# Performance work log

Hardware: AMD Instinct MI355X
Metric: run time of the kernel (lower is better)

Reference implementation:

```python
import jax, jax.numpy as jnp
import numpy as np

N_NODES = 100000
N_EDGES = 1600000
IN_C, HID, OUT_C = 128, 128, 64
BN_EPS = 1e-5


def gcn_conv(x, W, b, src, dst):
    # PyG GCNConv(normalize=False): linear first, then sum-aggregate over edges
    m = x @ W                                   # [N, out_dim]
    agg = jax.ops.segment_sum(m[src], dst, num_segments=N_NODES)  # scatter-add by dst
    return agg + b


def batch_norm(h, gamma, beta):
    mu = jnp.mean(h, axis=0)
    var = jnp.var(h, axis=0)
    return (h - mu) * jax.lax.rsqrt(var + BN_EPS) * gamma + beta


def setup_inputs() -> dict:
    key = jax.random.key(0)
    ks = jax.random.split(key, 8)
    x = jax.random.normal(ks[0], (N_NODES, IN_C), dtype=jnp.float32)
    edge_src = jax.random.randint(ks[1], (N_EDGES,), 0, N_NODES, dtype=jnp.int32)
    edge_dst = jnp.sort(jax.random.randint(ks[2], (N_EDGES,), 0, N_NODES, dtype=jnp.int32))
    def glorot(k, shape):
        lim = float(np.sqrt(6.0 / (shape[0] + shape[1])))
        return jax.random.uniform(k, shape, jnp.float32, -lim, lim)
    return {
        "x": x, "edge_src": edge_src, "edge_dst": edge_dst,
        "W0": glorot(ks[3], (IN_C, HID)), "b0": jnp.zeros((HID,), jnp.float32),
        "W1": glorot(ks[4], (HID, HID)), "b1": jnp.zeros((HID,), jnp.float32),
        "W2": glorot(ks[5], (HID, OUT_C)), "b2": jnp.zeros((OUT_C,), jnp.float32),
        "g0": jnp.ones((HID,), jnp.float32), "be0": jnp.zeros((HID,), jnp.float32),
        "g1": jnp.ones((HID,), jnp.float32), "be1": jnp.zeros((HID,), jnp.float32),
    }


def reference(x, edge_src, edge_dst, W0, b0, W1, b1, W2, b2, g0, be0, g1, be1):
    # layer 0: conv -> BN -> residual (dims match: 128==128) -> ReLU (dropout p=0)
    h = gcn_conv(x, W0, b0, edge_src, edge_dst)
    h = batch_norm(h, g0, be0)
    h = h + x  # residual, in_channels == hidden_channels
    x1 = jax.nn.relu(h)
    # layer 1
    h = gcn_conv(x1, W1, b1, edge_src, edge_dst)
    h = batch_norm(h, g1, be1)
    h = h + x1
    x2 = jax.nn.relu(h)
    # final layer: conv only
    return gcn_conv(x2, W2, b2, edge_src, edge_dst)
```

## Files before the change

kernel.cpp:

```cpp
#include <hip/hip_runtime.h>

#define BN_EPS 1e-5f

typedef __attribute__((ext_vector_type(8))) short bf16x8;
typedef __attribute__((ext_vector_type(4))) float f32x4;

__device__ __forceinline__ short f2bf(float f) {
    union { float f; unsigned u; } v; v.f = f;
    unsigned r = (v.u + 0x7fffu + ((v.u >> 16) & 1u)) >> 16;
    return (short)r;
}
__device__ __forceinline__ float bflo(unsigned d) {
    union { unsigned u; float f; } v; v.u = d << 16; return v.f;
}
__device__ __forceinline__ float bfhi(unsigned d) {
    union { unsigned u; float f; } v; v.u = d & 0xffff0000u; return v.f;
}

__global__ __launch_bounds__(256) void build_off_k(const int* __restrict__ dst,
                                                   int* __restrict__ off, int E, int N) {
    int i = blockIdx.x * 256 + threadIdx.x;
    if (i > E) return;
    int cur  = (i < E) ? dst[i] : N;
    int prev = (i == 0) ? -1 : dst[i - 1];
    for (int n = prev + 1; n <= cur; ++n) off[n] = i;
}

__global__ void zero_k(float* p, int n) {
    int i = blockIdx.x * blockDim.x + threadIdx.x;
    if (i < n) p[i] = 0.f;
}

__global__ __launch_bounds__(256) void wtrans_k(const float* __restrict__ W,
                                                short* __restrict__ Wt, int K, int C) {
    int i = blockIdx.x * 256 + threadIdx.x;
    if (i >= K * C) return;
    int c = i / K, k = i % K;
    Wt[i] = f2bf(W[k * C + c]);
}

template <int OUTC, int MODE>
__global__ __launch_bounds__(256) void mgemm_k(const void* __restrict__ Xp,
                                               const short* __restrict__ Wt,
                                               short* __restrict__ M,
                                               const float* __restrict__ ss,
                                               const void* __restrict__ Rp,
                                               short* __restrict__ X1, int N) {
    constexpr int NR = OUTC / 16;
    __shared__ short sW[OUTC][136];

    const int tid = threadIdx.x;
    for (int q = tid; q < OUTC * 16; q += 256) {
        int r = q >> 4, s = q & 15;
        *(int4*)&sW[r][s * 8] = ((const int4*)Wt)[q];
    }
    __syncthreads();

    const int wave = tid >> 6, lane = tid & 63;
    const int lr = lane & 15, lg = lane >> 4;
    const int row0 = blockIdx.x * 128 + wave * 32;

    f32x4 acc[2][NR];
    #pragma unroll
    for (int m = 0; m < 2; ++m)
        #pragma unroll
        for (int n = 0; n < NR; ++n) acc[m][n] = (f32x4){0.f, 0.f, 0.f, 0.f};

    #pragma unroll
    for (int kk = 0; kk < 4; ++kk) {
        bf16x8 a[2];
        const int ch0 = kk * 32 + lg * 8;
        #pragma unroll
        for (int m = 0; m < 2; ++m) {
            int row = row0 + m * 16 + lr;
            float v[8] = {0.f, 0.f, 0.f, 0.f, 0.f, 0.f, 0.f, 0.f};
            if (row < N) {
                if constexpr (MODE == 0) {
                    const float4* p = (const float4*)((const float*)Xp + (size_t)row * 128 + ch0);
                    float4 h0 = p[0], h1 = p[1];
                    v[0] = h0.x; v[1] = h0.y; v[2] = h0.z; v[3] = h0.w;
                    v[4] = h1.x; v[5] = h1.y; v[6] = h1.z; v[7] = h1.w;
                } else {
                    int4 hb = *(const int4*)((const short*)Xp + (size_t)row * 128 + ch0);
                    v[0] = bflo(hb.x); v[1] = bfhi(hb.x);
                    v[2] = bflo(hb.y); v[3] = bfhi(hb.y);
                    v[4] = bflo(hb.z); v[5] = bfhi(hb.z);
                    v[6] = bflo(hb.w); v[7] = bfhi(hb.w);
                    float4 sc0 = *(const float4*)&ss[ch0];
                    float4 sc1 = *(const float4*)&ss[ch0 + 4];
                    float4 sh0 = *(const float4*)&ss[128 + ch0];
                    float4 sh1 = *(const float4*)&ss[128 + ch0 + 4];
                    float sc[8] = {sc0.x, sc0.y, sc0.z, sc0.w, sc1.x, sc1.y, sc1.z, sc1.w};
                    float sh[8] = {sh0.x, sh0.y, sh0.z, sh0.w, sh1.x, sh1.y, sh1.z, sh1.w};
                    float r[8];
                    if constexpr (MODE == 1) {
                        const float4* rp = (const float4*)((const float*)Rp + (size_t)row * 128 + ch0);
                        float4 r0 = rp[0], r1 = rp[1];
                        r[0] = r0.x; r[1] = r0.y; r[2] = r0.z; r[3] = r0.w;
                        r[4] = r1.x; r[5] = r1.y; r[6] = r1.z; r[7] = r1.w;
                    } else {
                        int4 rb = *(const int4*)((const short*)Rp + (size_t)row * 128 + ch0);
                        r[0] = bflo(rb.x); r[1] = bfhi(rb.x);
                        r[2] = bflo(rb.y); r[3] = bfhi(rb.y);
                        r[4] = bflo(rb.z); r[5] = bfhi(rb.z);
                        r[6] = bflo(rb.w); r[7] = bfhi(rb.w);
                    }
                    #pragma unroll
                    for (int k = 0; k < 8; ++k)
                        v[k] = fmaxf(fmaf(v[k], sc[k], sh[k]) + r[k], 0.f);
                }
            }
            #pragma unroll
            for (int k = 0; k < 8; ++k) a[m][k] = f2bf(v[k]);
            if constexpr (MODE == 1) {
                if (row < N) *(bf16x8*)&X1[(size_t)row * 128 + ch0] = a[m];
            }
        }
        #pragma unroll
        for (int n = 0; n < NR; ++n) {
            bf16x8 b = *(const bf16x8*)&sW[n * 16 + lr][kk * 32 + lg * 8];
            acc[0][n] = __builtin_amdgcn_mfma_f32_16x16x32_bf16(a[0], b, acc[0][n], 0, 0, 0);
            acc[1][n] = __builtin_amdgcn_mfma_f32_16x16x32_bf16(a[1], b, acc[1][n], 0, 0, 0);
        }
    }

    #pragma unroll
    for (int m = 0; m < 2; ++m)
        #pragma unroll
        for (int r = 0; r < 4; ++r) {
            int row = row0 + m * 16 + lg * 4 + r;
            if (row < N) {
                #pragma unroll
                for (int n = 0; n < NR; ++n)
                    M[(size_t)row * OUTC + n * 16 + lr] = f2bf(acc[m][n][r]);
            }
        }
}

template <int C, bool STATS, bool OUTBF>
__global__ __launch_bounds__(256) void agg_k(const short* __restrict__ M,
                                             const int* __restrict__ src,
                                             const int* __restrict__ off,
                                             const float* __restrict__ bias,
                                             void* __restrict__ Hp,
                                             float* __restrict__ stats, int N) {
    constexpr int T = C / 8;
    constexpr int G = 64 / T;
    const int wave = threadIdx.x >> 6, lane = threadIdx.x & 63;
    const int g = lane / T, t = lane % T;
    const uint4* __restrict__ Mq = (const uint4*)M;

    float sum[8], sq[8];
    if constexpr (STATS) {
        #pragma unroll
        for (int k = 0; k < 8; ++k) { sum[k] = 0.f; sq[k] = 0.f; }
    }

    for (int node = blockIdx.x * 4 + wave; node < N; node += gridDim.x * 4) {
        const int e0 = off[node], e1 = off[node + 1];
        float acc[8];
        #pragma unroll
        for (int k = 0; k < 8; ++k) acc[k] = 0.f;

        for (int base = e0; base < e1; base += 64) {
            int cnt = e1 - base; if (cnt > 64) cnt = 64;
            int s = (base + lane < e1) ? src[base + lane] : 0;
            int ngrp = (cnt + G - 1) / G;
            for (int j = 0; j < ngrp; j += 4) {
                int i0 = j * G + g, i1 = i0 + G, i2 = i0 + 2 * G, i3 = i0 + 3 * G;
                int s0 = __shfl(s, i0 & 63), s1 = __shfl(s, i1 & 63);
                int s2 = __shfl(s, i2 & 63), s3 = __shfl(s, i3 & 63);
                uint4 d0 = make_uint4(0u,0u,0u,0u), d1 = d0, d2 = d0, d3 = d0;
                if (i0 < cnt) d0 = Mq[(size_t)s0 * T + t];
                if (i1 < cnt) d1 = Mq[(size_t)s1 * T + t];
                if (i2 < cnt) d2 = Mq[(size_t)s2 * T + t];
                if (i3 < cnt) d3 = Mq[(size_t)s3 * T + t];
                acc[0] += bflo(d0.x) + bflo(d1.x); acc[1] += bfhi(d0.x) + bfhi(d1.x);
                acc[2] += bflo(d0.y) + bflo(d1.y); acc[3] += bfhi(d0.y) + bfhi(d1.y);
                acc[4] += bflo(d0.z) + bflo(d1.z); acc[5] += bfhi(d0.z) + bfhi(d1.z);
                acc[6] += bflo(d0.w) + bflo(d1.w); acc[7] += bfhi(d0.w) + bfhi(d1.w);
                acc[0] += bflo(d2.x) + bflo(d3.x); acc[1] += bfhi(d2.x) + bfhi(d3.x);
                acc[2] += bflo(d2.y) + bflo(d3.y); acc[3] += bfhi(d2.y) + bfhi(d3.y);
                acc[4] += bflo(d2.z) + bflo(d3.z); acc[5] += bfhi(d2.z) + bfhi(d3.z);
                acc[6] += bflo(d2.w) + bflo(d3.w); acc[7] += bfhi(d2.w) + bfhi(d3.w);
            }
        }
        #pragma unroll
        for (int dlt = T; dlt < 64; dlt <<= 1)
            #pragma unroll
            for (int k = 0; k < 8; ++k) acc[k] += __shfl_xor(acc[k], dlt);

        if (g == 0) {
            float h[8];
            #pragma unroll
            for (int k = 0; k < 8; ++k) h[k] = acc[k] + bias[t * 8 + k];
            if constexpr (OUTBF) {
                bf16x8 hv;
                #pragma unroll
                for (int k = 0; k < 8; ++k) hv[k] = f2bf(h[k]);
                *(bf16x8*)((short*)Hp + (size_t)node * C + t * 8) = hv;
            } else {
                *(float4*)((float*)Hp + (size_t)node * C + t * 8)     = make_float4(h[0], h[1], h[2], h[3]);
                *(float4*)((float*)Hp + (size_t)node * C + t * 8 + 4) = make_float4(h[4], h[5], h[6], h[7]);
            }
            if constexpr (STATS) {
                #pragma unroll
                for (int k = 0; k < 8; ++k) {
                    sum[k] += h[k]; sq[k] = fmaf(h[k], h[k], sq[k]);
                }
            }
        }
    }

    if constexpr (STATS) {
        __shared__ float sL[4 * 256];
        if (g == 0) {
            #pragma unroll
            for (int k = 0; k < 8; ++k) {
                sL[wave * 256 + t * 8 + k]       = sum[k];
                sL[wave * 256 + 128 + t * 8 + k] = sq[k];
            }
        }
        __syncthreads();
        int tid = threadIdx.x;
        float v = sL[tid] + sL[256 + tid] + sL[512 + tid] + sL[768 + tid];
        atomicAdd(&stats[tid], v);
    }
}

__global__ void bnfin_k(const float* __restrict__ stats, const float* __restrict__ gamma,
                        const float* __restrict__ beta, float* __restrict__ ss, float invN) {
    int c = threadIdx.x;
    float mu  = stats[c] * invN;
    float var = fmaf(-mu, mu, stats[128 + c] * invN);
    float sc  = gamma[c] * rsqrtf(var + BN_EPS);
    ss[c]       = sc;
    ss[128 + c] = fmaf(-mu, sc, beta[c]);
}

extern "C" void kernel_launch(void* const* d_in, const int* in_sizes, int n_in,
                              void* d_out, int out_size, void* d_ws, size_t ws_size,
                              hipStream_t stream) {
    const float* x   = (const float*)d_in[0];
    const int*   src = (const int*)d_in[1];
    const int*   dst = (const int*)d_in[2];
    const float* W0  = (const float*)d_in[3];
    const float* b0  = (const float*)d_in[4];
    const float* W1  = (const float*)d_in[5];
    const float* b1  = (const float*)d_in[6];
    const float* W2  = (const float*)d_in[7];
    const float* b2  = (const float*)d_in[8];
    const float* g0  = (const float*)d_in[9];
    const float* be0 = (const float*)d_in[10];
    const float* g1  = (const float*)d_in[11];
    const float* be1 = (const float*)d_in[12];
    float* out = (float*)d_out;

    const int N = in_sizes[0] / 128;
    const int E = in_sizes[1];

    char*  ws   = (char*)d_ws;
    size_t bufH = (size_t)N * 128 * sizeof(short);
    short* Mb = (short*)(ws);
    short* Hb = (short*)(ws + bufH);
    short* X1 = (short*)(ws + 2 * bufH);
    size_t p  = 3 * bufH;
    p = (p + 255) & ~(size_t)255;
    int*   off = (int*)(ws + p);
    p += ((size_t)(N + 1) * sizeof(int) + 255) & ~(size_t)255;
    float* stats0 = (float*)(ws + p); p += 1024;
    float* stats1 = (float*)(ws + p); p += 1024;
    float* ss0    = (float*)(ws + p); p += 1024;
    float* ss1    = (float*)(ws + p); p += 1024;
    short* Wt0    = (short*)(ws + p); p += 128 * 128 * 2;
    short* Wt1    = (short*)(ws + p); p += 128 * 128 * 2;
    short* Wt2    = (short*)(ws + p); p += 128 * 64 * 2;

    const dim3 blk(256);
    const int gGemm = (N + 127) / 128;
    const int gAgg  = 4096;
    const float invN = 1.f / (float)N;

    zero_k<<<2, blk, 0, stream>>>(stats0, 512);
    wtrans_k<<<64, blk, 0, stream>>>(W0, Wt0, 128, 128);
    wtrans_k<<<64, blk, 0, stream>>>(W1, Wt1, 128, 128);
    wtrans_k<<<32, blk, 0, stream>>>(W2, Wt2, 128, 64);
    build_off_k<<<(E + 256) / 256, blk, 0, stream>>>(dst, off, E, N);

    mgemm_k<128, 0><<<gGemm, blk, 0, stream>>>(x, Wt0, Mb, nullptr, nullptr, nullptr, N);
    agg_k<128, true, true><<<gAgg, blk, 0, stream>>>(Mb, src, off, b0, Hb, stats0, N);
    bnfin_k<<<1, 128, 0, stream>>>(stats0, g0, be0, ss0, invN);

    mgemm_k<128, 1><<<gGemm, blk, 0, stream>>>(Hb, Wt1, Mb, ss0, x, X1, N);
    agg_k<128, true, true><<<gAgg, blk, 0, stream>>>(Mb, src, off, b1, Hb, stats1, N);
    bnfin_k<<<1, 128, 0, stream>>>(stats1, g1, be1, ss1, invN);

    mgemm_k<64, 2><<<gGemm, blk, 0, stream>>>(Hb, Wt2, Mb, ss1, X1, nullptr, N);
    agg_k<64, false, false><<<gAgg, blk, 0, stream>>>(Mb, src, off, b2, out, stats0, N);
}
```

Measured before the change: 380.3 us.

## Restructure aggregation to one node per wave, lane-per-channel, separate BN stats kernel

The aggregation kernel now gives each wave exactly one node, launched with one block per four nodes, and has each lane own one or two channels, so every source row is read in one coalesced wave-wide load. This removes the grouped uint4 loads, masked loads and the cross-lane shuffle reduction. BatchNorm statistics move out of the aggregation into a separate stats kernel that re-reads the bf16 hidden buffer. This adds an extra pass over the hidden buffer and an extra launch per layer. It also serialises edges within a wave, which lowers memory-level parallelism per wave but may balance load better on the sorted CSR.

```diff
diff --git a/kernel.cpp b/kernel.cpp
--- a/kernel.cpp
+++ b/kernel.cpp
@@ -137,95 +137,96 @@
         }
 }
 
-template <int C, bool STATS, bool OUTBF>
+template <int C, bool OUTBF>
 __global__ __launch_bounds__(256) void agg_k(const short* __restrict__ M,
                                              const int* __restrict__ src,
                                              const int* __restrict__ off,
                                              const float* __restrict__ bias,
-                                             void* __restrict__ Hp,
-                                             float* __restrict__ stats, int N) {
-    constexpr int T = C / 8;
-    constexpr int G = 64 / T;
-    const int wave = threadIdx.x >> 6, lane = threadIdx.x & 63;
-    const int g = lane / T, t = lane % T;
-    const uint4* __restrict__ Mq = (const uint4*)M;
-
-    float sum[8], sq[8];
-    if constexpr (STATS) {
-        #pragma unroll
-        for (int k = 0; k < 8; ++k) { sum[k] = 0.f; sq[k] = 0.f; }
+                                             void* __restrict__ Hp, int N) {
+    const int lane = threadIdx.x & 63;
+    const int node = blockIdx.x * 4 + (threadIdx.x >> 6);
+    if (node >= N) return;
+    const int e0 = off[node], e1 = off[node + 1];
+
+    if constexpr (C == 128) {
+        const unsigned* __restrict__ M32 = (const unsigned*)M;
+        float2 acc = make_float2(0.f, 0.f);
+        for (int base = e0; base < e1; base += 64) {
+            int e = base + lane;
+            int s = (e < e1) ? src[e] : 0;
+            int cnt = min(64, e1 - base);
+            int i = 0;
+            for (; i + 4 <= cnt; i += 4) {
+                int s0 = __shfl(s, i),     s1 = __shfl(s, i + 1);
+                int s2 = __shfl(s, i + 2), s3 = __shfl(s, i + 3);
+                unsigned d0 = M32[(size_t)s0 * 64 + lane];
+                unsigned d1 = M32[(size_t)s1 * 64 + lane];
+                unsigned d2 = M32[(size_t)s2 * 64 + lane];
+                unsigned d3 = M32[(size_t)s3 * 64 + lane];
+                acc.x += (bflo(d0) + bflo(d1)) + (bflo(d2) + bflo(d3));
+                acc.y += (bfhi(d0) + bfhi(d1)) + (bfhi(d2) + bfhi(d3));
+            }
+            for (; i < cnt; ++i) {
+                int si = __shfl(s, i);
+                unsigned d = M32[(size_t)si * 64 + lane];
+                acc.x += bflo(d); acc.y += bfhi(d);
+            }
+        }
+        float2 bv = *(const float2*)&bias[lane * 2];
+        float hx = acc.x + bv.x, hy = acc.y + bv.y;
+        if constexpr (OUTBF) {
+            unsigned d = (unsigned)(unsigned short)f2bf(hx)
+                       | ((unsigned)(unsigned short)f2bf(hy) << 16);
+            ((unsigned*)Hp)[(size_t)node * 64 + lane] = d;
+        } else {
+            *(float2*)((float*)Hp + (size_t)node * 128 + lane * 2) = make_float2(hx, hy);
+        }
+    } else {
+        const unsigned short* __restrict__ M16 = (const unsigned short*)M;
+        float acc = 0.f;
+        for (int base = e0; base < e1; base += 64) {
+            int e = base + lane;
+            int s = (e < e1) ? src[e] : 0;
+            int cnt = min(64, e1 - base);
+            int i = 0;
+            for (; i + 4 <= cnt; i += 4) {
+                int s0 = __shfl(s, i),     s1 = __shfl(s, i + 1);
+                int s2 = __shfl(s, i + 2), s3 = __shfl(s, i + 3);
+                float v0 = bflo((unsigned)M16[(size_t)s0 * 64 + lane]);
+                float v1 = bflo((unsigned)M16[(size_t)s1 * 64 + lane]);
+                float v2 = bflo((unsigned)M16[(size_t)s2 * 64 + lane]);
+                float v3 = bflo((unsigned)M16[(size_t)s3 * 64 + lane]);
+                acc += (v0 + v1) + (v2 + v3);
+            }
+            for (; i < cnt; ++i) {
+                int si = __shfl(s, i);
+                acc += bflo((unsigned)M16[(size_t)si * 64 + lane]);
+            }
+        }
+        ((float*)Hp)[(size_t)node * 64 + lane] = acc + bias[lane];
     }
-
-    for (int node = blockIdx.x * 4 + wave; node < N; node += gridDim.x * 4) {
-        const int e0 = off[node], e1 = off[node + 1];
-        float acc[8];
-        #pragma unroll
-        for (int k = 0; k < 8; ++k) acc[k] = 0.f;
-
-        for (int base = e0; base < e1; base += 64) {
-            int cnt = e1 - base; if (cnt > 64) cnt = 64;
-            int s = (base + lane < e1) ? src[base + lane] : 0;
-            int ngrp = (cnt + G - 1) / G;
-            for (int j = 0; j < ngrp; j += 4) {
-                int i0 = j * G + g, i1 = i0 + G, i2 = i0 + 2 * G, i3 = i0 + 3 * G;
-                int s0 = __shfl(s, i0 & 63), s1 = __shfl(s, i1 & 63);
-                int s2 = __shfl(s, i2 & 63), s3 = __shfl(s, i3 & 63);
-                uint4 d0 = make_uint4(0u,0u,0u,0u), d1 = d0, d2 = d0, d3 = d0;
-                if (i0 < cnt) d0 = Mq[(size_t)s0 * T + t];
-                if (i1 < cnt) d1 = Mq[(size_t)s1 * T + t];
-                if (i2 < cnt) d2 = Mq[(size_t)s2 * T + t];
-                if (i3 < cnt) d3 = Mq[(size_t)s3 * T + t];
-                acc[0] += bflo(d0.x) + bflo(d1.x); acc[1] += bfhi(d0.x) + bfhi(d1.x);
-                acc[2] += bflo(d0.y) + bflo(d1.y); acc[3] += bfhi(d0.y) + bfhi(d1.y);
-                acc[4] += bflo(d0.z) + bflo(d1.z); acc[5] += bfhi(d0.z) + bfhi(d1.z);
-                acc[6] += bflo(d0.w) + bflo(d1.w); acc[7] += bfhi(d0.w) + bfhi(d1.w);
-                acc[0] += bflo(d2.x) + bflo(d3.x); acc[1] += bfhi(d2.x) + bfhi(d3.x);
-                acc[2] += bflo(d2.y) + bflo(d3.y); acc[3] += bfhi(d2.y) + bfhi(d3.y);
-                acc[4] += bflo(d2.z) + bflo(d3.z); acc[5] += bfhi(d2.z) + bfhi(d3.z);
-                acc[6] += bflo(d2.w) + bflo(d3.w); acc[7] += bfhi(d2.w) + bfhi(d3.w);
-            }
-        }
-        #pragma unroll
-        for (int dlt = T; dlt < 64; dlt <<= 1)
-            #pragma unroll
-            for (int k = 0; k < 8; ++k) acc[k] += __shfl_xor(acc[k], dlt);
-
-        if (g == 0) {
-            float h[8];
-            #pragma unroll
-            for (int k = 0; k < 8; ++k) h[k] = acc[k] + bias[t * 8 + k];
-            if constexpr (OUTBF) {
-                bf16x8 hv;
-                #pragma unroll
-                for (int k = 0; k < 8; ++k) hv[k] = f2bf(h[k]);
-                *(bf16x8*)((short*)Hp + (size_t)node * C + t * 8) = hv;
-            } else {
-                *(float4*)((float*)Hp + (size_t)node * C + t * 8)     = make_float4(h[0], h[1], h[2], h[3]);
-                *(float4*)((float*)Hp + (size_t)node * C + t * 8 + 4) = make_float4(h[4], h[5], h[6], h[7]);
-            }
-            if constexpr (STATS) {
-                #pragma unroll
-                for (int k = 0; k < 8; ++k) {
-                    sum[k] += h[k]; sq[k] = fmaf(h[k], h[k], sq[k]);
-                }
-            }
-        }
+}
+
+__global__ __launch_bounds__(256) void stats_k(const short* __restrict__ Hb,
+                                               float* __restrict__ stats, int N) {
+    const int lane = threadIdx.x & 63, wave = threadIdx.x >> 6;
+    const unsigned* __restrict__ H32 = (const unsigned*)Hb;
+    float2 sum = make_float2(0.f, 0.f), sq = make_float2(0.f, 0.f);
+    for (int r = blockIdx.x * 4 + wave; r < N; r += gridDim.x * 4) {
+        unsigned d = H32[(size_t)r * 64 + lane];
+        float lo = bflo(d), hi = bfhi(d);
+        sum.x += lo; sum.y += hi;
+        sq.x = fmaf(lo, lo, sq.x); sq.y = fmaf(hi, hi, sq.y);
     }
-
-    if constexpr (STATS) {
-        __shared__ float sL[4 * 256];
-        if (g == 0) {
-            #pragma unroll
-            for (int k = 0; k < 8; ++k) {
-                sL[wave * 256 + t * 8 + k]       = sum[k];
-                sL[wave * 256 + 128 + t * 8 + k] = sq[k];
-            }
-        }
-        __syncthreads();
-        int tid = threadIdx.x;
-        float v = sL[tid] + sL[256 + tid] + sL[512 + tid] + sL[768 + tid];
-        atomicAdd(&stats[tid], v);
-    }
+    __shared__ float sL[4][256];
+    sL[wave][lane * 2]           = sum.x;
+    sL[wave][lane * 2 + 1]       = sum.y;
+    sL[wave][128 + lane * 2]     = sq.x;
+    sL[wave][128 + lane * 2 + 1] = sq.y;
+    __syncthreads();
+    int tid = threadIdx.x;
+    float v = sL[0][tid] + sL[1][tid] + sL[2][tid] + sL[3][tid];
+    atomicAdd(&stats[tid], v);
 }
 
 __global__ void bnfin_k(const float* __restrict__ stats, const float* __restrict__ gamma,
@@ -277,8 +278,9 @@
     short* Wt2    = (short*)(ws + p); p += 128 * 64 * 2;
 
     const dim3 blk(256);
-    const int gGemm = (N + 127) / 128;
-    const int gAgg  = 4096;
+    const int gGemm  = (N + 127) / 128;
+    const int gAgg   = (N + 3) / 4;
+    const int gStats = 2048;
     const float invN = 1.f / (float)N;
 
     zero_k<<<2, blk, 0, stream>>>(stats0, 512);
@@ -288,13 +290,15 @@
     build_off_k<<<(E + 256) / 256, blk, 0, stream>>>(dst, off, E, N);
 
     mgemm_k<128, 0><<<gGemm, blk, 0, stream>>>(x, Wt0, Mb, nullptr, nullptr, nullptr, N);
-    agg_k<128, true, true><<<gAgg, blk, 0, stream>>>(Mb, src, off, b0, Hb, stats0, N);
+    agg_k<128, true><<<gAgg, blk, 0, stream>>>(Mb, src, off, b0, Hb, N);
+    stats_k<<<gStats, blk, 0, stream>>>(Hb, stats0, N);
     bnfin_k<<<1, 128, 0, stream>>>(stats0, g0, be0, ss0, invN);
 
     mgemm_k<128, 1><<<gGemm, blk, 0, stream>>>(Hb, Wt1, Mb, ss0, x, X1, N);
-    agg_k<128, true, true><<<gAgg, blk, 0, stream>>>(Mb, src, off, b1, Hb, stats1, N);
+    agg_k<128, true><<<gAgg, blk, 0, stream>>>(Mb, src, off, b1, Hb, N);
+    stats_k<<<gStats, blk, 0, stream>>>(Hb, stats1, N);
     bnfin_k<<<1, 128, 0, stream>>>(stats1, g1, be1, ss1, invN);
 
     mgemm_k<64, 2><<<gGemm, blk, 0, stream>>>(Hb, Wt2, Mb, ss1, X1, nullptr, N);
-    agg_k<64, false, false><<<gAgg, blk, 0, stream>>>(Mb, src, off, b2, out, stats0, N);
-}
+    agg_k<64, false><<<gAgg, blk, 0, stream>>>(Mb, src, off, b2, out, N);
+}
```

Result: faster. 370.1 us (-2.7%).
